# Optimization experiments

Hardware: AMD Instinct MI355X
Metric: run time of the kernel (lower is better)

Reference implementation:

```python
import jax, jax.numpy as jnp
import numpy as np

N_NODES = 50000
N_EDGES = 800000
D_IN = 128
D_OUT = 128


def setup_inputs() -> dict:
    key = jax.random.key(0)
    k1, k2, k3, k4, k5, k6 = jax.random.split(key, 6)
    feat = jax.random.normal(k1, (N_NODES, D_IN), dtype=jnp.float32)
    src = jax.random.randint(k2, (N_EDGES,), 0, N_NODES, dtype=jnp.int64)
    dst = jax.random.randint(k3, (N_EDGES,), 0, N_NODES, dtype=jnp.int64)
    # Glorot-like scale for the linear weights (fc_neigh has no bias; fc_self has bias)
    scale = 1.0 / np.sqrt(D_IN)
    W_neigh = jax.random.normal(k4, (D_OUT, D_IN), dtype=jnp.float32) * scale
    W_self = jax.random.normal(k5, (D_OUT, D_IN), dtype=jnp.float32) * scale
    b_self = jax.random.normal(k6, (D_OUT,), dtype=jnp.float32) * scale
    return {"feat": feat, "src": src, "dst": dst,
            "W_neigh": W_neigh, "W_self": W_self, "b_self": b_self}


def reference(feat, src, dst, W_neigh, W_self, b_self):
    """SAGEConv with aggregator_type='mean', feat_drop=0, bias=True.

    in_feats == out_feats (128) -> lin_before_mp is False:
      h_neigh = fc_neigh(mean over incoming neighbors of feat)
      out     = fc_self(feat) + h_neigh
    """
    n = feat.shape[0]
    # message passing: copy_u + fn.mean('m', 'neigh')
    msgs = feat[src]                                            # [E, D_in]
    summed = jax.ops.segment_sum(msgs, dst, num_segments=n)     # [N, D_in]
    deg = jax.ops.segment_sum(jnp.ones((src.shape[0],), feat.dtype),
                              dst, num_segments=n)              # [N]
    # zero in-degree -> neigh = 0 (matches DGL mean semantics)
    h_neigh = summed / jnp.maximum(deg, 1.0)[:, None]
    h_neigh = h_neigh @ W_neigh.T                               # fc_neigh (no bias)
    h_self = feat @ W_self.T + b_self                           # fc_self (bias)
    return h_self + h_neigh
```

## Files before the change

kernel.cpp:

```cpp
#include <hip/hip_runtime.h>
#include <hip/hip_bf16.h>

typedef __hip_bfloat16 bf16;
typedef __attribute__((ext_vector_type(8))) short bf16x8;
typedef __attribute__((ext_vector_type(4))) float f32x4;
#define DIM 128
#define BK 64
#define PCAP 4096
#define CHUNK 4096
#define EPT 16

__device__ __forceinline__ float bfbits(unsigned short u) {
    return __uint_as_float(((unsigned)u) << 16);
}
__device__ __forceinline__ unsigned short f2bf(float f) {
    bf16 h = __float2bfloat16(f);
    return *(unsigned short*)&h;
}
__device__ __forceinline__ void load8(const void* p, int is32, size_t off, float* f) {
    if (is32) {
        const float* q = (const float*)p + off;
        float4 a = *(const float4*)q;
        float4 b = *(const float4*)(q + 4);
        f[0] = a.x; f[1] = a.y; f[2] = a.z; f[3] = a.w;
        f[4] = b.x; f[5] = b.y; f[6] = b.z; f[7] = b.w;
    } else {
        uint4 v = *(const uint4*)((const unsigned short*)p + off);
        const unsigned int* w = (const unsigned int*)&v;
#pragma unroll
        for (int i = 0; i < 4; i++) {
            f[2 * i]     = __uint_as_float(w[i] << 16);
            f[2 * i + 1] = __uint_as_float(w[i] & 0xffff0000u);
        }
    }
}
__device__ __forceinline__ int read_idx(const void* p, int is64, int e) {
    return is64 ? (int)((const long long*)p)[e] : ((const int*)p)[e];
}

__device__ __forceinline__ int is_fp32_wave(const unsigned int* p, int lane) {
    unsigned w = p[lane];
    unsigned low = w & 0xFFFFu;
    unsigned ex = (low >> 7) & 0xFFu;
    bool hit = (ex >= 90u && ex <= 140u) || low == 0u || low == 0x8000u;
    unsigned long long m = __ballot(hit);
    return (2 * __popcll(m) < 64) ? 1 : 0;
}
__global__ void init_kernel(const unsigned int* __restrict__ src,
                            const unsigned int* __restrict__ feat,
                            const unsigned int* __restrict__ wn,
                            const unsigned int* __restrict__ wsm,
                            const unsigned int* __restrict__ bias,
                            int* __restrict__ flags, int* __restrict__ cnt, int Z) {
    int i = blockIdx.x * blockDim.x + threadIdx.x;
    if (i < Z) cnt[i] = 0;
    if (blockIdx.x == 0 && threadIdx.x < 64) {
        int lane = threadIdx.x;
        unsigned long long m = __ballot(src[1 + 2 * lane] != 0u);
        int f1 = is_fp32_wave(feat, lane);
        int f2 = is_fp32_wave(wn, lane);
        int f3 = is_fp32_wave(wsm, lane);
        int f4 = is_fp32_wave(bias, lane);
        if (lane == 0) {
            flags[0] = (m == 0ull) ? 1 : 0;
            flags[1] = f1; flags[2] = f2; flags[3] = f3; flags[4] = f4;
        }
    }
}

__global__ __launch_bounds__(256) void part_kernel(
    const void* __restrict__ srcv, const void* __restrict__ dstv,
    const int* __restrict__ flags, int* __restrict__ gcnt,
    unsigned* __restrict__ pbuf,
    const float* __restrict__ featf, unsigned short* __restrict__ wsbf,
    int E, int N, int eblocks, int total8, int nparts, int cstride) {
    __shared__ int hist[1024];
    __shared__ int bstart[1024];
    __shared__ int gbase[1024];
    __shared__ int tsum[256];
    __shared__ unsigned stage[CHUNK];

    int b = blockIdx.x;
    int t = threadIdx.x;

    if (b >= eblocks) {
        if (!flags[1]) return;
        for (int i = (b - eblocks) * 256 + t; i < total8; i += cstride) {
            size_t e = (size_t)i * 8;
            float4 a = *(const float4*)(featf + e);
            float4 bb = *(const float4*)(featf + e + 4);
            unsigned short u[8] = {f2bf(a.x), f2bf(a.y), f2bf(a.z), f2bf(a.w),
                                   f2bf(bb.x), f2bf(bb.y), f2bf(bb.z), f2bf(bb.w)};
            *(uint4*)(wsbf + e) = *(uint4*)u;
        }
        return;
    }

    int is64 = flags[0];
    for (int i = t; i < nparts; i += 256) hist[i] = 0;
    __syncthreads();

    unsigned v[EPT];
    int base = b * CHUNK;
#pragma unroll
    for (int j = 0; j < EPT; j++) {
        int e = base + j * 256 + t;
        unsigned val = 0xFFFFFFFFu;
        if (e < E) {
            int s = read_idx(srcv, is64, e);
            int d = read_idx(dstv, is64, e);
            if ((unsigned)s < (unsigned)N && (unsigned)d < (unsigned)N)
                val = ((unsigned)d << 16) | (unsigned)s;
        }
        v[j] = val;
        if (val != 0xFFFFFFFFu) atomicAdd(&hist[val >> 22], 1);
    }
    __syncthreads();

    int K = (nparts + 255) >> 8;
    int s0 = 0;
    for (int j = 0; j < K; j++) {
        int bin = t * K + j;
        if (bin < nparts) s0 += hist[bin];
    }
    tsum[t] = s0;
    __syncthreads();
    for (int off = 1; off < 256; off <<= 1) {
        int x = (t >= off) ? tsum[t - off] : 0;
        __syncthreads();
        tsum[t] += x;
        __syncthreads();
    }
    int tot = tsum[255];
    int run = (t > 0) ? tsum[t - 1] : 0;
    for (int j = 0; j < K; j++) {
        int bin = t * K + j;
        if (bin < nparts) {
            bstart[bin] = run;
            int h = hist[bin];
            run += h;
            gbase[bin] = h ? atomicAdd(&gcnt[bin], h) : 0;
        }
    }
    __syncthreads();
    for (int i = t; i < nparts; i += 256) hist[i] = bstart[i];
    __syncthreads();

#pragma unroll
    for (int j = 0; j < EPT; j++) {
        unsigned val = v[j];
        if (val != 0xFFFFFFFFu) {
            int bin = val >> 22;
            int p = atomicAdd(&hist[bin], 1);
            stage[p] = val;
        }
    }
    __syncthreads();

    for (int p = t; p < tot; p += 256) {
        unsigned val = stage[p];
        int bin = val >> 22;
        unsigned off = (unsigned)(gbase[bin] + (p - bstart[bin]));
        if (off < PCAP) pbuf[(size_t)bin * PCAP + off] = val;
    }
}

__global__ __launch_bounds__(256) void fused_kernel(
    const void* __restrict__ feat, const unsigned short* __restrict__ wsbf,
    const unsigned* __restrict__ pbuf, const int* __restrict__ gcnt,
    void* __restrict__ dout, int N, const int* __restrict__ flags) {
    __shared__ int cnt[16];
    __shared__ unsigned short list[16][64];

    int t = threadIdx.x;
    int p = blockIdx.x >> 2;
    int qq = blockIdx.x & 3;
    int nbase = p << 6;
    int feat32 = flags[1];
    const unsigned short* sb = feat32 ? wsbf : (const unsigned short*)feat;

    if (t < 16) cnt[t] = 0;
    __syncthreads();

    int ec = gcnt[p];
    if (ec > PCAP) ec = PCAP;
    for (int i = t; i < ec; i += 256) {
        unsigned val = pbuf[(size_t)p * PCAP + i];
        int local = (int)(val >> 16) - nbase;
        if ((local >> 4) == qq) {
            int pos = atomicAdd(&cnt[local & 15], 1);
            if (pos < 64) list[local & 15][pos] = (unsigned short)(val & 0xFFFFu);
        }
    }
    __syncthreads();

    int lane = t & 63;
    int wv = t >> 6;
    int grp = lane >> 4;
    int li = lane & 15;

    for (int q = 0; q < 4; q++) {
        int l16 = wv * 4 + q;
        int node = nbase + (qq << 4) + l16;
        if (node >= N) break;
        int deg = cnt[l16];
        int use = deg < 64 ? deg : 64;

        float acc[8];
#pragma unroll
        for (int i = 0; i < 8; i++) acc[i] = 0.f;

        for (int k = 0; k < use; k += 16) {
            uint4 v[4];
            float wgt[4];
#pragma unroll
            for (int j = 0; j < 4; j++) {
                int r = k + j * 4 + grp;
                wgt[j] = (r < use) ? 1.0f : 0.0f;
                int rc = (r < use) ? r : (use - 1);
                int s = list[l16][rc];
                v[j] = *(const uint4*)(sb + (size_t)s * DIM + li * 8);
            }
#pragma unroll
            for (int j = 0; j < 4; j++) {
                const unsigned* w = (const unsigned*)&v[j];
#pragma unroll
                for (int i = 0; i < 4; i++) {
                    acc[2 * i]     = fmaf(wgt[j], __uint_as_float(w[i] << 16), acc[2 * i]);
                    acc[2 * i + 1] = fmaf(wgt[j], __uint_as_float(w[i] & 0xffff0000u), acc[2 * i + 1]);
                }
            }
        }

#pragma unroll
        for (int i = 0; i < 8; i++) {
            acc[i] += __shfl_xor(acc[i], 16);
            acc[i] += __shfl_xor(acc[i], 32);
        }

        float rd = 1.0f / fmaxf((float)deg, 1.0f);
        if (grp == 0) {
            unsigned short u[8];
#pragma unroll
            for (int i = 0; i < 8; i++) u[i] = f2bf(acc[i] * rd);
            size_t ob = feat32 ? ((size_t)node * 512 + 256 + (size_t)li * 16)
                               : ((size_t)node * 256 + (size_t)li * 16);
            *(uint4*)((char*)dout + ob) = *(uint4*)u;
        }
    }
}

__global__ void buckcvt_kernel(const void* __restrict__ srcv, const void* __restrict__ dstv,
                               const int* __restrict__ flags, int* __restrict__ cnt,
                               unsigned short* __restrict__ b16, int* __restrict__ b32,
                               const float* __restrict__ featf,
                               unsigned short* __restrict__ wsbf,
                               int E, int N, int eblocks, int total8, int use16, int ws_ok) {
    int b = blockIdx.x;
    if (b < eblocks) {
        int e = b * 256 + threadIdx.x;
        if (e >= E) return;
        int is64 = flags[0];
        int s = read_idx(srcv, is64, e);
        int d = read_idx(dstv, is64, e);
        if ((unsigned)s >= (unsigned)N || (unsigned)d >= (unsigned)N) return;
        int pos = atomicAdd(&cnt[d], 1);
        if (pos < BK) {
            if (use16) b16[(size_t)d * BK + pos] = (unsigned short)s;
            else       b32[(size_t)d * BK + pos] = s;
        }
    } else {
        if (!flags[1] || !ws_ok) return;
        int i = (b - eblocks) * 256 + threadIdx.x;
        if (i >= total8) return;
        size_t e = (size_t)i * 8;
        float4 a = *(const float4*)(featf + e);
        float4 bb = *(const float4*)(featf + e + 4);
        unsigned short u[8] = {f2bf(a.x), f2bf(a.y), f2bf(a.z), f2bf(a.w),
                               f2bf(bb.x), f2bf(bb.y), f2bf(bb.z), f2bf(bb.w)};
        *(uint4*)(wsbf + e) = *(uint4*)u;
    }
}

__global__ __launch_bounds__(256) void gather_kernel(
    const void* __restrict__ feat, const unsigned short* __restrict__ wsbf,
    const unsigned short* __restrict__ b16, const int* __restrict__ b32,
    const int* __restrict__ cnt, void* __restrict__ dout,
    int N, const int* __restrict__ flags, int use16, int ws_ok) {
    int t = threadIdx.x;
    int lane = t & 63;
    int wv = t >> 6;
    int node = blockIdx.x * 4 + wv;
    if (node >= N) return;
    int feat32 = flags[1];
    int bfmode = (!feat32) || ws_ok;
    const unsigned short* sb = feat32 ? wsbf : (const unsigned short*)feat;
    const float* ff = (const float*)feat;

    int deg = __builtin_amdgcn_readfirstlane(cnt[node]);
    int use = deg < BK ? deg : BK;
    int idxv;
    if (use16) idxv = b16[(size_t)node * BK + (lane < use ? lane : 0)];
    else       idxv = b32[(size_t)node * BK + (lane < use ? lane : 0)];

    float a0 = 0.f, a1 = 0.f;
    int k = 0;
    if (bfmode) {
        for (; k + 8 <= use; k += 8) {
            int ss[8];
#pragma unroll
            for (int j = 0; j < 8; j++) ss[j] = __shfl(idxv, k + j);
            unsigned uu[8];
#pragma unroll
            for (int j = 0; j < 8; j++)
                uu[j] = *(const unsigned*)(sb + (size_t)ss[j] * DIM + lane * 2);
#pragma unroll
            for (int j = 0; j < 8; j++) {
                a0 += bfbits((unsigned short)uu[j]);
                a1 += bfbits((unsigned short)(uu[j] >> 16));
            }
        }
        for (; k < use; k++) {
            int s = __shfl(idxv, k);
            unsigned u = *(const unsigned*)(sb + (size_t)s * DIM + lane * 2);
            a0 += bfbits((unsigned short)u);
            a1 += bfbits((unsigned short)(u >> 16));
        }
    } else {
        for (; k + 4 <= use; k += 4) {
            int s0 = __shfl(idxv, k),     s1 = __shfl(idxv, k + 1);
            int s2 = __shfl(idxv, k + 2), s3 = __shfl(idxv, k + 3);
            float2 v0 = *(const float2*)(ff + (size_t)s0 * DIM + lane * 2);
            float2 v1 = *(const float2*)(ff + (size_t)s1 * DIM + lane * 2);
            float2 v2 = *(const float2*)(ff + (size_t)s2 * DIM + lane * 2);
            float2 v3 = *(const float2*)(ff + (size_t)s3 * DIM + lane * 2);
            a0 += (v0.x + v1.x) + (v2.x + v3.x);
            a1 += (v0.y + v1.y) + (v2.y + v3.y);
        }
        for (; k < use; k++) {
            int s = __shfl(idxv, k);
            float2 v = *(const float2*)(ff + (size_t)s * DIM + lane * 2);
            a0 += v.x; a1 += v.y;
        }
    }

    float rd = 1.0f / fmaxf((float)deg, 1.0f);
    unsigned up = ((unsigned)f2bf(a1 * rd) << 16) | (unsigned)f2bf(a0 * rd);
    size_t ob = feat32 ? ((size_t)node * 512 + 256 + (size_t)lane * 4)
                       : ((size_t)node * 256 + (size_t)lane * 4);
    *(unsigned*)((char*)dout + ob) = up;
}

#define TPW 2
__global__ __launch_bounds__(256) void gemm_kernel(
    const void* __restrict__ feat, const unsigned short* __restrict__ wsbf,
    const void* __restrict__ Wn, const void* __restrict__ Ws,
    const void* __restrict__ bias, void* __restrict__ out,
    int N, const int* __restrict__ flags, int ws_ok) {
    __shared__ short ldsb[4096 * 8];

    int t = threadIdx.x;
    int lane = t & 63;
    int wv = t >> 6;
    int feat32 = flags[1], wn32 = flags[2], ws32 = flags[3], bs32 = flags[4];
    int bfmode = (!feat32) || ws_ok;

    for (int f = t; f < 4096; f += 256) {
        int tj = f >> 9, ks = (f >> 6) & 7, ln = f & 63;
        int j = tj * 16 + (ln & 15);
        int kk = ks * 32 + (ln >> 4) * 8;
        float w[8];
        if (kk < DIM) load8(Ws, ws32, (size_t)j * DIM + kk, w);
        else          load8(Wn, wn32, (size_t)j * DIM + (kk - DIM), w);
        unsigned short u[8];
#pragma unroll
        for (int i = 0; i < 8; i++) u[i] = f2bf(w[i]);
        *(uint4*)(ldsb + (size_t)f * 8) = *(uint4*)u;
    }
    __syncthreads();

    const bf16x8* bfrag = (const bf16x8*)ldsb;

    float bcol[8];
#pragma unroll
    for (int tj = 0; tj < 8; tj++) {
        int col = tj * 16 + (lane & 15);
        bcol[tj] = bs32 ? ((const float*)bias)[col]
                        : bfbits(((const unsigned short*)bias)[col]);
    }

    int quad = lane >> 4;
    int NT = (N + 15) >> 4;
    int gw = blockIdx.x * 4 + wv;

    const unsigned short* sb = feat32 ? wsbf : (const unsigned short*)feat;
    const char* hbase = (const char*)out;
    size_t hrow = feat32 ? 512 : 256;
    size_t hoff = feat32 ? 256 : 0;

    int tile0 = gw * TPW;
    int tile1 = tile0 + 1;
    if (tile0 >= NT) return;
    int has1 = (tile1 < NT);
    int tb0 = tile0 * 16;
    int tb1 = has1 ? tile1 * 16 : tb0;

    int arow0 = tb0 + (lane & 15); if (arow0 >= N) arow0 = N - 1;
    int arow1 = tb1 + (lane & 15); if (arow1 >= N) arow1 = N - 1;

    bf16x8 afr0[8], afr1[8];
#pragma unroll
    for (int ks = 0; ks < 4; ks++) {
        int kk = ks * 32 + quad * 8;
        if (bfmode) {
            afr0[ks] = *(const bf16x8*)(sb + (size_t)arow0 * DIM + kk);
            afr1[ks] = *(const bf16x8*)(sb + (size_t)arow1 * DIM + kk);
        } else {
            float av[8]; unsigned short u[8];
            load8(feat, 1, (size_t)arow0 * DIM + kk, av);
#pragma unroll
            for (int i = 0; i < 8; i++) u[i] = f2bf(av[i]);
            afr0[ks] = *(bf16x8*)u;
            load8(feat, 1, (size_t)arow1 * DIM + kk, av);
#pragma unroll
            for (int i = 0; i < 8; i++) u[i] = f2bf(av[i]);
            afr1[ks] = *(bf16x8*)u;
        }
    }
#pragma unroll
    for (int ks = 4; ks < 8; ks++) {
        int kk = (ks - 4) * 32 + quad * 8;
        afr0[ks] = *(const bf16x8*)(hbase + (size_t)arow0 * hrow + hoff + (size_t)kk * 2);
        afr1[ks] = *(const bf16x8*)(hbase + (size_t)arow1 * hrow + hoff + (size_t)kk * 2);
    }

    f32x4 acc0[8], acc1[8];
#pragma unroll
    for (int tj = 0; tj < 8; tj++) {
        acc0[tj] = (f32x4){bcol[tj], bcol[tj], bcol[tj], bcol[tj]};
        acc1[tj] = acc0[tj];
    }

#pragma unroll
    for (int tj = 0; tj < 8; tj++) {
#pragma unroll
        for (int ks = 0; ks < 8; ks++) {
            bf16x8 bf = bfrag[(tj * 8 + ks) * 64 + lane];
            acc0[tj] = __builtin_amdgcn_mfma_f32_16x16x32_bf16(afr0[ks], bf, acc0[tj], 0, 0, 0);
            acc1[tj] = __builtin_amdgcn_mfma_f32_16x16x32_bf16(afr1[ks], bf, acc1[tj], 0, 0, 0);
        }
    }

#pragma unroll
    for (int tj = 0; tj < 8; tj++) {
        int col = tj * 16 + (lane & 15);
#pragma unroll
        for (int r = 0; r < 4; r++) {
            int row0 = tb0 + quad * 4 + r;
            if (row0 < N) {
                size_t idx = (size_t)row0 * DIM + col;
                if (feat32) ((float*)out)[idx] = acc0[tj][r];
                else ((unsigned short*)out)[idx] = f2bf(acc0[tj][r]);
            }
            if (has1) {
                int row1 = tb1 + quad * 4 + r;
                if (row1 < N) {
                    size_t idx = (size_t)row1 * DIM + col;
                    if (feat32) ((float*)out)[idx] = acc1[tj][r];
                    else ((unsigned short*)out)[idx] = f2bf(acc1[tj][r]);
                }
            }
        }
    }
}

extern "C" void kernel_launch(void* const* d_in, const int* in_sizes, int n_in,
                              void* d_out, int out_size, void* d_ws, size_t ws_size,
                              hipStream_t stream) {
    const void* feat = d_in[0];
    const void* src  = d_in[1];
    const void* dst  = d_in[2];
    const void* Wn   = d_in[3];
    const void* Ws   = d_in[4];
    const void* bias = d_in[5];

    const int N = in_sizes[0] / DIM;
    const int E = in_sizes[1];
    const int use16 = (N <= 65535) ? 1 : 0;
    const int total8 = N * DIM / 8;
    int* flags = (int*)d_ws;

    const int nparts = (N + 63) >> 6;
    size_t pbuf_off = (64 + (size_t)nparts * 4 + 255) & ~(size_t)255;
    size_t wsf_off  = (pbuf_off + (size_t)nparts * PCAP * 4 + 255) & ~(size_t)255;
    size_t need_f   = wsf_off + (size_t)N * DIM * 2;
    const int FAST = (use16 && nparts <= 1024 && ws_size >= need_f) ? 1 : 0;

    if (FAST) {
        int* gcnt = (int*)((char*)d_ws + 64);
        unsigned* pbuf = (unsigned*)((char*)d_ws + pbuf_off);
        unsigned short* wsbf = (unsigned short*)((char*)d_ws + wsf_off);

        init_kernel<<<(nparts + 255) / 256, 256, 0, stream>>>(
            (const unsigned int*)src, (const unsigned int*)feat, (const unsigned int*)Wn,
            (const unsigned int*)Ws, (const unsigned int*)bias, flags, gcnt, nparts);

        int eb = (E + CHUNK - 1) / CHUNK;
        int cb = (total8 + 255) / 256;
        if (cb > 1024) cb = 1024;
        part_kernel<<<eb + cb, 256, 0, stream>>>(
            src, dst, flags, gcnt, pbuf, (const float*)feat, wsbf,
            E, N, eb, total8, nparts, cb * 256);

        fused_kernel<<<nparts * 4, 256, 0, stream>>>(
            feat, wsbf, pbuf, gcnt, d_out, N, flags);

        int NT = (N + 15) / 16;
        int gwaves = (NT + TPW - 1) / TPW;
        gemm_kernel<<<(gwaves + 3) / 4, 256, 0, stream>>>(
            feat, wsbf, Wn, Ws, bias, d_out, N, flags, 1);
        return;
    }

    const size_t esz = use16 ? 2 : 4;
    int* cnt = flags + 16;
    unsigned short* b16 = (unsigned short*)(cnt + N);
    int* b32 = (int*)(cnt + N);
    size_t bucket_bytes = (size_t)N * BK * esz;
    size_t bf_off = (64 + (size_t)N * 4 + bucket_bytes + 15) & ~(size_t)15;
    unsigned short* wsbf = (unsigned short*)((char*)d_ws + bf_off);
    size_t need = bf_off + (size_t)N * DIM * 2;
    int ws_ok = (ws_size >= need) ? 1 : 0;

    init_kernel<<<(N + 255) / 256, 256, 0, stream>>>(
        (const unsigned int*)src, (const unsigned int*)feat, (const unsigned int*)Wn,
        (const unsigned int*)Ws, (const unsigned int*)bias, flags, cnt, N);

    int eblocks = (E + 255) / 256;
    int cblocks = ws_ok ? (total8 + 255) / 256 : 0;
    buckcvt_kernel<<<eblocks + cblocks, 256, 0, stream>>>(
        src, dst, flags, cnt, b16, b32, (const float*)feat, wsbf,
        E, N, eblocks, total8, use16, ws_ok);

    gather_kernel<<<(N + 3) / 4, 256, 0, stream>>>(
        feat, wsbf, b16, b32, cnt, d_out, N, flags, use16, ws_ok);

    int NT = (N + 15) / 16;
    int gwaves = (NT + TPW - 1) / TPW;
    gemm_kernel<<<(gwaves + 3) / 4, 256, 0, stream>>>(
        feat, wsbf, Wn, Ws, bias, d_out, N, flags, ws_ok);
}
```

Measured before the change: 160.0 us.

## Fuse neighbor aggregation with MFMA GEMM and widen partition blocks to 1024

The neighbor-mean gather and the dense GEMM now run in one kernel. Each block handles 64 nodes: it builds the adjacency lists, aggregates the neighbors, stages both weight matrices as bf16 in LDS, and runs the MFMA projection plus bias. This drops a kernel launch and keeps the aggregated rows close to the block that reuses them. In exchange, every block reloads and converts the full weights, uses 64KB of LDS, and the gather runs with fewer blocks, which may lower occupancy. The partition kernel also moves to 1024-thread blocks so each thread owns one histogram bin and the scan is simpler.

```diff
diff --git a/kernel.cpp b/kernel.cpp
--- a/kernel.cpp
+++ b/kernel.cpp
@@ -8,7 +8,7 @@
 #define BK 64
 #define PCAP 4096
 #define CHUNK 4096
-#define EPT 16
+#define EPT2 4
 
 __device__ __forceinline__ float bfbits(unsigned short u) {
     return __uint_as_float(((unsigned)u) << 16);
@@ -68,7 +68,7 @@
     }
 }
 
-__global__ __launch_bounds__(256) void part_kernel(
+__global__ __launch_bounds__(1024) void part_kernel(
     const void* __restrict__ srcv, const void* __restrict__ dstv,
     const int* __restrict__ flags, int* __restrict__ gcnt,
     unsigned* __restrict__ pbuf,
@@ -77,7 +77,7 @@
     __shared__ int hist[1024];
     __shared__ int bstart[1024];
     __shared__ int gbase[1024];
-    __shared__ int tsum[256];
+    __shared__ int tsum[1024];
     __shared__ unsigned stage[CHUNK];
 
     int b = blockIdx.x;
@@ -85,7 +85,7 @@
 
     if (b >= eblocks) {
         if (!flags[1]) return;
-        for (int i = (b - eblocks) * 256 + t; i < total8; i += cstride) {
+        for (int i = (b - eblocks) * 1024 + t; i < total8; i += cstride) {
             size_t e = (size_t)i * 8;
             float4 a = *(const float4*)(featf + e);
             float4 bb = *(const float4*)(featf + e + 4);
@@ -97,14 +97,14 @@
     }
 
     int is64 = flags[0];
-    for (int i = t; i < nparts; i += 256) hist[i] = 0;
-    __syncthreads();
-
-    unsigned v[EPT];
+    hist[t] = 0;
+    __syncthreads();
+
+    unsigned v[EPT2];
     int base = b * CHUNK;
 #pragma unroll
-    for (int j = 0; j < EPT; j++) {
-        int e = base + j * 256 + t;
+    for (int j = 0; j < EPT2; j++) {
+        int e = base + j * 1024 + t;
         unsigned val = 0xFFFFFFFFu;
         if (e < E) {
             int s = read_idx(srcv, is64, e);
@@ -117,69 +117,66 @@
     }
     __syncthreads();
 
-    int K = (nparts + 255) >> 8;
-    int s0 = 0;
-    for (int j = 0; j < K; j++) {
-        int bin = t * K + j;
-        if (bin < nparts) s0 += hist[bin];
-    }
-    tsum[t] = s0;
-    __syncthreads();
-    for (int off = 1; off < 256; off <<= 1) {
+    int h = (t < nparts) ? hist[t] : 0;
+    tsum[t] = h;
+    __syncthreads();
+    for (int off = 1; off < 1024; off <<= 1) {
         int x = (t >= off) ? tsum[t - off] : 0;
         __syncthreads();
         tsum[t] += x;
         __syncthreads();
     }
-    int tot = tsum[255];
+    int tot = tsum[1023];
     int run = (t > 0) ? tsum[t - 1] : 0;
-    for (int j = 0; j < K; j++) {
-        int bin = t * K + j;
-        if (bin < nparts) {
-            bstart[bin] = run;
-            int h = hist[bin];
-            run += h;
-            gbase[bin] = h ? atomicAdd(&gcnt[bin], h) : 0;
-        }
-    }
-    __syncthreads();
-    for (int i = t; i < nparts; i += 256) hist[i] = bstart[i];
-    __syncthreads();
-
-#pragma unroll
-    for (int j = 0; j < EPT; j++) {
+    if (t < nparts) {
+        bstart[t] = run;
+        hist[t] = run;
+        gbase[t] = h ? atomicAdd(&gcnt[t], h) : 0;
+    }
+    __syncthreads();
+
+#pragma unroll
+    for (int j = 0; j < EPT2; j++) {
         unsigned val = v[j];
         if (val != 0xFFFFFFFFu) {
             int bin = val >> 22;
-            int p = atomicAdd(&hist[bin], 1);
-            stage[p] = val;
-        }
-    }
-    __syncthreads();
-
-    for (int p = t; p < tot; p += 256) {
-        unsigned val = stage[p];
+            int pos = atomicAdd(&hist[bin], 1);
+            stage[pos] = val;
+        }
+    }
+    __syncthreads();
+
+    for (int pp = t; pp < tot; pp += 1024) {
+        unsigned val = stage[pp];
         int bin = val >> 22;
-        unsigned off = (unsigned)(gbase[bin] + (p - bstart[bin]));
+        unsigned off = (unsigned)(gbase[bin] + (pp - bstart[bin]));
         if (off < PCAP) pbuf[(size_t)bin * PCAP + off] = val;
     }
 }
 
-__global__ __launch_bounds__(256) void fused_kernel(
+__global__ __launch_bounds__(256) void ggemm_kernel(
     const void* __restrict__ feat, const unsigned short* __restrict__ wsbf,
     const unsigned* __restrict__ pbuf, const int* __restrict__ gcnt,
-    void* __restrict__ dout, int N, const int* __restrict__ flags) {
-    __shared__ int cnt[16];
-    __shared__ unsigned short list[16][64];
+    const void* __restrict__ Wn, const void* __restrict__ Ws,
+    const void* __restrict__ bias, void* __restrict__ out,
+    int N, const int* __restrict__ flags) {
+    __shared__ short ldsb[4096 * 8];
+
+    int* cntp = (int*)ldsb;
+    unsigned short (*list)[64] = (unsigned short (*)[64])(ldsb + 128);
 
     int t = threadIdx.x;
-    int p = blockIdx.x >> 2;
-    int qq = blockIdx.x & 3;
+    int lane = t & 63;
+    int wv = t >> 6;
+    int p = blockIdx.x;
     int nbase = p << 6;
-    int feat32 = flags[1];
+    int feat32 = flags[1], wn32 = flags[2], ws32 = flags[3], bs32 = flags[4];
     const unsigned short* sb = feat32 ? wsbf : (const unsigned short*)feat;
-
-    if (t < 16) cnt[t] = 0;
+    char* hbase = (char*)out;
+    size_t hrow = feat32 ? 512 : 256;
+    size_t hoff = feat32 ? 256 : 0;
+
+    if (t < 64) cntp[t] = 0;
     __syncthreads();
 
     int ec = gcnt[p];
@@ -187,23 +184,18 @@
     for (int i = t; i < ec; i += 256) {
         unsigned val = pbuf[(size_t)p * PCAP + i];
         int local = (int)(val >> 16) - nbase;
-        if ((local >> 4) == qq) {
-            int pos = atomicAdd(&cnt[local & 15], 1);
-            if (pos < 64) list[local & 15][pos] = (unsigned short)(val & 0xFFFFu);
-        }
-    }
-    __syncthreads();
-
-    int lane = t & 63;
-    int wv = t >> 6;
+        int pos = atomicAdd(&cntp[local], 1);
+        if (pos < 64) list[local][pos] = (unsigned short)(val & 0xFFFFu);
+    }
+    __syncthreads();
+
     int grp = lane >> 4;
     int li = lane & 15;
-
-    for (int q = 0; q < 4; q++) {
-        int l16 = wv * 4 + q;
-        int node = nbase + (qq << 4) + l16;
+    for (int q = 0; q < 16; q++) {
+        int local = wv * 16 + q;
+        int node = nbase + local;
         if (node >= N) break;
-        int deg = cnt[l16];
+        int deg = cntp[local];
         int use = deg < 64 ? deg : 64;
 
         float acc[8];
@@ -218,7 +210,7 @@
                 int r = k + j * 4 + grp;
                 wgt[j] = (r < use) ? 1.0f : 0.0f;
                 int rc = (r < use) ? r : (use - 1);
-                int s = list[l16][rc];
+                int s = list[local][rc];
                 v[j] = *(const uint4*)(sb + (size_t)s * DIM + li * 8);
             }
 #pragma unroll
@@ -231,21 +223,87 @@
                 }
             }
         }
-
 #pragma unroll
         for (int i = 0; i < 8; i++) {
             acc[i] += __shfl_xor(acc[i], 16);
             acc[i] += __shfl_xor(acc[i], 32);
         }
-
         float rd = 1.0f / fmaxf((float)deg, 1.0f);
         if (grp == 0) {
             unsigned short u[8];
 #pragma unroll
             for (int i = 0; i < 8; i++) u[i] = f2bf(acc[i] * rd);
-            size_t ob = feat32 ? ((size_t)node * 512 + 256 + (size_t)li * 16)
-                               : ((size_t)node * 256 + (size_t)li * 16);
-            *(uint4*)((char*)dout + ob) = *(uint4*)u;
+            *(uint4*)(hbase + (size_t)node * hrow + hoff + (size_t)li * 16) = *(uint4*)u;
+        }
+    }
+    __syncthreads();
+
+    for (int f = t; f < 4096; f += 256) {
+        int tj = f >> 9, ks = (f >> 6) & 7, ln = f & 63;
+        int j = tj * 16 + (ln & 15);
+        int kk = ks * 32 + (ln >> 4) * 8;
+        float w[8];
+        if (kk < DIM) load8(Ws, ws32, (size_t)j * DIM + kk, w);
+        else          load8(Wn, wn32, (size_t)j * DIM + (kk - DIM), w);
+        unsigned short u[8];
+#pragma unroll
+        for (int i = 0; i < 8; i++) u[i] = f2bf(w[i]);
+        *(uint4*)(ldsb + (size_t)f * 8) = *(uint4*)u;
+    }
+    __syncthreads();
+
+    const bf16x8* bfrag = (const bf16x8*)ldsb;
+    int quad = lane >> 4;
+
+    float bcol[8];
+#pragma unroll
+    for (int tj = 0; tj < 8; tj++) {
+        int col = tj * 16 + (lane & 15);
+        bcol[tj] = bs32 ? ((const float*)bias)[col]
+                        : bfbits(((const unsigned short*)bias)[col]);
+    }
+
+    int tb = nbase + wv * 16;
+    int arow = tb + (lane & 15);
+    if (arow >= N) arow = N - 1;
+
+    bf16x8 afr[8];
+#pragma unroll
+    for (int ks = 0; ks < 4; ks++) {
+        int kk = ks * 32 + quad * 8;
+        afr[ks] = *(const bf16x8*)(sb + (size_t)arow * DIM + kk);
+    }
+#pragma unroll
+    for (int ks = 4; ks < 8; ks++) {
+        int kk = (ks - 4) * 32 + quad * 8;
+        afr[ks] = *(const bf16x8*)(hbase + (size_t)arow * hrow + hoff + (size_t)kk * 2);
+    }
+
+    f32x4 acc[8];
+#pragma unroll
+    for (int tj = 0; tj < 8; tj++)
+        acc[tj] = (f32x4){bcol[tj], bcol[tj], bcol[tj], bcol[tj]};
+
+#pragma unroll
+    for (int tj = 0; tj < 8; tj++) {
+#pragma unroll
+        for (int ks = 0; ks < 8; ks++) {
+            acc[tj] = __builtin_amdgcn_mfma_f32_16x16x32_bf16(
+                afr[ks], bfrag[(tj * 8 + ks) * 64 + lane], acc[tj], 0, 0, 0);
+        }
+    }
+
+#pragma unroll
+    for (int tj = 0; tj < 8; tj++) {
+        int col = tj * 16 + (lane & 15);
+#pragma unroll
+        for (int r = 0; r < 4; r++) {
+            int row = tb + quad * 4 + r;
+            if (row < N) {
+                size_t idx = (size_t)row * DIM + col;
+                if (feat32) ((float*)out)[idx] = acc[tj][r];
+                else ((unsigned short*)out)[idx] = f2bf(acc[tj][r]);
+            }
         }
     }
 }
@@ -506,19 +564,14 @@
             (const unsigned int*)Ws, (const unsigned int*)bias, flags, gcnt, nparts);
 
         int eb = (E + CHUNK - 1) / CHUNK;
-        int cb = (total8 + 255) / 256;
+        int cb = (total8 + 1023) / 1024;
         if (cb > 1024) cb = 1024;
-        part_kernel<<<eb + cb, 256, 0, stream>>>(
+        part_kernel<<<eb + cb, 1024, 0, stream>>>(
             src, dst, flags, gcnt, pbuf, (const float*)feat, wsbf,
-            E, N, eb, total8, nparts, cb * 256);
-
-        fused_kernel<<<nparts * 4, 256, 0, stream>>>(
-            feat, wsbf, pbuf, gcnt, d_out, N, flags);
-
-        int NT = (N + 15) / 16;
-        int gwaves = (NT + TPW - 1) / TPW;
-        gemm_kernel<<<(gwaves + 3) / 4, 256, 0, stream>>>(
-            feat, wsbf, Wn, Ws, bias, d_out, N, flags, 1);
+            E, N, eb, total8, nparts, cb * 1024);
+
+        ggemm_kernel<<<nparts, 256, 0, stream>>>(
+            feat, wsbf, pbuf, gcnt, Wn, Ws, bias, d_out, N, flags);
         return;
     }
 
```

Result: no change. 160.8 us (+0.5%).
